# Performance work log

Measured on AMD Instinct MI355X. Metric: run time of the kernel, lower is better.

## Reference

```python
import jax, jax.numpy as jnp
import numpy as np
from jax import lax

DIM = 256
HEAD_DIM = 64          # v head dim and hedgehog dim
HEAD_DIM_QK = 64       # must equal HEAD_DIM for the module to run
NH = DIM // HEAD_DIM   # 4
EPS = 1e-6


def setup_inputs() -> dict:
    key = jax.random.key(0)
    ks = jax.random.split(key, 12)
    B, C, H, W, D = 1, DIM, 16, 16, 16
    x = jax.random.normal(ks[0], (B, C, H, W, D), dtype=jnp.float32)
    qk_dim = HEAD_DIM_QK * NH
    # 1x1x1 conv weights for q, k (qkv_bias=False)
    Wq = jax.random.normal(ks[1], (qk_dim, C), dtype=jnp.float32) * 0.02
    Wk = jax.random.normal(ks[2], (qk_dim, C), dtype=jnp.float32) * 0.02
    # depthwise 3x3x3 conv for v (groups=dim, bias=True)
    Wv = jax.random.normal(ks[3], (C, 1, 3, 3, 3), dtype=jnp.float32) * 0.1
    bv = jax.random.normal(ks[4], (C,), dtype=jnp.float32) * 0.02
    # HedgeHog linear layers (init is identity/zeros; use near-identity + noise)
    eye = jnp.eye(HEAD_DIM, dtype=jnp.float32)
    Wmq = eye * 0.5 + jax.random.normal(ks[5], (HEAD_DIM, HEAD_DIM), dtype=jnp.float32) * 0.02
    bmq = jnp.zeros((HEAD_DIM,), dtype=jnp.float32)
    Wmk = eye * 0.5 + jax.random.normal(ks[6], (HEAD_DIM, HEAD_DIM), dtype=jnp.float32) * 0.02
    bmk = jnp.zeros((HEAD_DIM,), dtype=jnp.float32)
    Wmv = eye * 0.5 + jax.random.normal(ks[7], (HEAD_DIM, HEAD_DIM), dtype=jnp.float32) * 0.02
    bmv = jnp.zeros((HEAD_DIM,), dtype=jnp.float32)
    return {"x": x, "Wq": Wq, "Wk": Wk, "Wv": Wv, "bv": bv,
            "Wmq": Wmq, "bmq": bmq, "Wmk": Wmk, "bmk": bmk,
            "Wmv": Wmv, "bmv": bmv}


def _hedgehog(z, W, b):
    # z: [B, nh, N, d] -> [B, 2*nh, N, d]; cat along HEAD axis (dim=1) as in torch code
    h = jnp.einsum('bhnd,ed->bhne', z, W) + b
    return jnp.concatenate([jnp.exp(h), jnp.exp(-h)], axis=1)


def reference(x, Wq, Wk, Wv, bv, Wmq, bmq, Wmk, bmk, Wmv, bmv):
    B, C, H, W_, D = x.shape
    N = H * W_ * D
    x2 = x.reshape(B, C, N)
    # 1x1x1 conv projections
    q = jnp.einsum('oc,bcn->bon', Wq, x2)  # [B, qk_dim, N]
    k = jnp.einsum('oc,bcn->bon', Wk, x2)
    # depthwise 3x3x3 conv for v
    v3 = lax.conv_general_dilated(
        x, Wv, window_strides=(1, 1, 1),
        padding=((1, 1), (1, 1), (1, 1)),
        dimension_numbers=('NCDHW', 'OIDHW', 'NCDHW'),
        feature_group_count=C) + bv[None, :, None, None, None]
    v = v3.reshape(B, C, N)
    # split heads, tokens-last -> tokens axis
    q1 = q.reshape(B, NH, HEAD_DIM_QK, N).transpose(0, 1, 3, 2)  # [B,nh,N,dqk]
    k1 = k.reshape(B, NH, HEAD_DIM_QK, N).transpose(0, 1, 3, 2)
    v1 = v.reshape(B, NH, HEAD_DIM, N).transpose(0, 1, 3, 2)     # [B,nh,N,dv]
    qf = _hedgehog(q1, Wmq, bmq)  # [B,2nh,N,dqk]
    kf = _hedgehog(k1, Wmk, bmk)
    vf = _hedgehog(v1, Wmv, bmv)  # [B,2nh,N,dv]
    # quadratic "linear" attention: row-sum normalized QK^T
    qk = jnp.einsum('bhmd,bhnd->bhmn', qf, kf)          # [B,2nh,N,N]
    attn = qk / (jnp.sum(qk, axis=-1, keepdims=True) + EPS)
    out = jnp.einsum('bhmn,bhnd->bhmd', attn, vf)        # [B,2nh,N,dv]
    out = out.transpose(0, 1, 3, 2).reshape(B, 2 * C, H, W_, D)
    return out
```

## Files before the change

kernel.cpp:

```cpp
#include <hip/hip_runtime.h>
#include <math.h>

#define EPS_F 1e-6f

#define OFF_WCQ 0
#define OFF_WCK (OFF_WCQ + 65536)
#define OFF_BV  (OFF_WCK + 65536)
#define OFF_VC  (OFF_BV + 256)
#define OFF_PS  (OFF_VC + 256*4096)
#define OFF_PSV (OFF_PS + 8*64*4096)
#define OFF_SM  (OFF_PSV + 8*64*64)
#define OFF_SV  (OFF_SM + 8*4096)

__global__ __launch_bounds__(256) void k_combine(
    const float* __restrict__ Wq, const float* __restrict__ Wk,
    const float* __restrict__ Wmq, const float* __restrict__ Wmk,
    const float* __restrict__ Wmv, const float* __restrict__ bmv,
    const float* __restrict__ bv, float* __restrict__ ws)
{
    int row = blockIdx.x;
    int c = threadIdx.x;
    int h = row >> 6, e = row & 63;
    float aq = 0.f, ak = 0.f;
    for (int d = 0; d < 64; ++d) {
        float mq = Wmq[e*64 + d];
        float mk = Wmk[e*64 + d];
        int src = (h*64 + d)*256 + c;
        aq = fmaf(mq, Wq[src], aq);
        ak = fmaf(mk, Wk[src], ak);
    }
    ws[OFF_WCQ + row*256 + c] = aq;
    ws[OFF_WCK + row*256 + c] = ak;
    if (c == 0) {
        float av = 0.f;
        for (int d = 0; d < 64; ++d) av = fmaf(Wmv[e*64 + d], bv[h*64 + d], av);
        ws[OFF_BV + row] = av + bmv[e];
    }
}

__global__ __launch_bounds__(256) void k_dwconv(
    const float* __restrict__ x, const float* __restrict__ Wv, float* __restrict__ vc)
{
    int c = blockIdx.y;
    int n = blockIdx.x * 256 + threadIdx.x;
    int z = n >> 8, y = (n >> 4) & 15, xx = n & 15;
    const float* xc = x + c * 4096;
    const float* wc = Wv + c * 27;
    float acc = 0.f;
    #pragma unroll
    for (int kz = 0; kz < 3; ++kz) {
        int zz = z + kz - 1;
        if (zz < 0 || zz > 15) continue;
        #pragma unroll
        for (int ky = 0; ky < 3; ++ky) {
            int yy = y + ky - 1;
            if (yy < 0 || yy > 15) continue;
            #pragma unroll
            for (int kx = 0; kx < 3; ++kx) {
                int xv = xx + kx - 1;
                if (xv < 0 || xv > 15) continue;
                acc = fmaf(wc[(kz*3 + ky)*3 + kx], xc[(zz << 8) + (yy << 4) + xv], acc);
            }
        }
    }
    vc[c*4096 + n] = acc;
}

__global__ __launch_bounds__(256, 1) void k_kv_fused(
    const float* __restrict__ X, const float* __restrict__ bmk,
    const float* __restrict__ Wmv, float* __restrict__ ws)
{
    __shared__ float smem[16384];
    float (*Xs)[64]  = (float(*)[64])smem;
    float (*Ws)[68]  = (float(*)[68])(smem + 4096);
    float (*kfp)[64] = (float(*)[64])smem;
    float (*kfm)[64] = (float(*)[64])(smem + 4096);
    float (*vfp)[64] = (float(*)[64])(smem + 8192);
    float (*vfm)[64] = (float(*)[64])(smem + 12288);

    int t = threadIdx.x;
    int chunk = blockIdx.x;
    int hb = blockIdx.y;
    int n0 = chunk * 64;
    int lc = t >> 6, ln = t & 63;
    int e4 = (t & 15) * 4;
    int n4 = (t >> 4) * 4;

    float accK[4][4], accV[4][4];
    #pragma unroll
    for (int i = 0; i < 4; ++i)
        #pragma unroll
        for (int j = 0; j < 4; ++j) { accK[i][j] = 0.f; accV[i][j] = 0.f; }

    const float* Wck = ws + OFF_WCK;
    for (int c0 = 0; c0 < 256; c0 += 64) {
        #pragma unroll
        for (int i = 0; i < 16; ++i)
            Xs[lc*16 + i][ln] = X[(size_t)(c0 + lc*16 + i)*4096 + n0 + ln];
        #pragma unroll
        for (int i = 0; i < 16; ++i)
            Ws[ln][lc*16 + i] = Wck[(size_t)(hb*64 + lc*16 + i)*256 + c0 + ln];
        __syncthreads();
        #pragma unroll 4
        for (int c = 0; c < 64; ++c) {
            float4 xv4 = *(const float4*)&Xs[c][n4];
            float4 wv4 = *(const float4*)&Ws[c][e4];
            float xv[4] = {xv4.x, xv4.y, xv4.z, xv4.w};
            float wv[4] = {wv4.x, wv4.y, wv4.z, wv4.w};
            #pragma unroll
            for (int ii = 0; ii < 4; ++ii)
                #pragma unroll
                for (int jj = 0; jj < 4; ++jj)
                    accK[ii][jj] = fmaf(xv[ii], wv[jj], accK[ii][jj]);
        }
        __syncthreads();
    }

    const float* vcb = ws + OFF_VC + (size_t)hb*64*4096;
    #pragma unroll
    for (int i = 0; i < 16; ++i)
        Xs[lc*16 + i][ln] = vcb[(size_t)(lc*16 + i)*4096 + n0 + ln];
    #pragma unroll
    for (int i = 0; i < 16; ++i) { int idx = i*256 + t; Ws[idx & 63][idx >> 6] = Wmv[idx]; }
    __syncthreads();
    #pragma unroll 4
    for (int d = 0; d < 64; ++d) {
        float4 xv4 = *(const float4*)&Xs[d][n4];
        float4 wv4 = *(const float4*)&Ws[d][e4];
        float xv[4] = {xv4.x, xv4.y, xv4.z, xv4.w};
        float wv[4] = {wv4.x, wv4.y, wv4.z, wv4.w};
        #pragma unroll
        for (int ii = 0; ii < 4; ++ii)
            #pragma unroll
            for (int jj = 0; jj < 4; ++jj)
                accV[ii][jj] = fmaf(xv[ii], wv[jj], accV[ii][jj]);
    }
    __syncthreads();

    float bk[4], bvv[4];
    #pragma unroll
    for (int j = 0; j < 4; ++j) { bk[j] = bmk[e4 + j]; bvv[j] = ws[OFF_BV + hb*64 + e4 + j]; }
    #pragma unroll
    for (int ii = 0; ii < 4; ++ii) {
        float pk[4], mk_[4], pv[4], mv[4];
        #pragma unroll
        for (int jj = 0; jj < 4; ++jj) {
            float a = accK[ii][jj] + bk[jj];
            pk[jj] = __expf(a);  mk_[jj] = __expf(-a);
            float b = accV[ii][jj] + bvv[jj];
            pv[jj] = __expf(b);  mv[jj] = __expf(-b);
        }
        *(float4*)&kfp[n4 + ii][e4] = make_float4(pk[0], pk[1], pk[2], pk[3]);
        *(float4*)&kfm[n4 + ii][e4] = make_float4(mk_[0], mk_[1], mk_[2], mk_[3]);
        *(float4*)&vfp[n4 + ii][e4] = make_float4(pv[0], pv[1], pv[2], pv[3]);
        *(float4*)&vfm[n4 + ii][e4] = make_float4(mv[0], mv[1], mv[2], mv[3]);
    }
    __syncthreads();

    float aSp[4][4], aSm[4][4], svp[4], svm[4];
    #pragma unroll
    for (int i = 0; i < 4; ++i) {
        svp[i] = 0.f; svm[i] = 0.f;
        #pragma unroll
        for (int j = 0; j < 4; ++j) { aSp[i][j] = 0.f; aSm[i][j] = 0.f; }
    }
    int a4 = e4, f4 = n4;
    #pragma unroll 2
    for (int n = 0; n < 64; ++n) {
        float4 kp4 = *(const float4*)&kfp[n][a4];
        float4 km4 = *(const float4*)&kfm[n][a4];
        float4 vp4 = *(const float4*)&vfp[n][f4];
        float4 vm4 = *(const float4*)&vfm[n][f4];
        float kp[4] = {kp4.x, kp4.y, kp4.z, kp4.w};
        float km[4] = {km4.x, km4.y, km4.z, km4.w};
        float vp[4] = {vp4.x, vp4.y, vp4.z, vp4.w};
        float vm[4] = {vm4.x, vm4.y, vm4.z, vm4.w};
        #pragma unroll
        for (int ai = 0; ai < 4; ++ai) {
            svp[ai] += kp[ai];  svm[ai] += km[ai];
            #pragma unroll
            for (int fi = 0; fi < 4; ++fi) {
                aSp[ai][fi] = fmaf(kp[ai], vp[fi], aSp[ai][fi]);
                aSm[ai][fi] = fmaf(km[ai], vm[fi], aSm[ai][fi]);
            }
        }
    }
    float* pSp = ws + OFF_PS + (size_t)(hb*64 + chunk)*4096;
    float* pSm = ws + OFF_PS + (size_t)((hb + 4)*64 + chunk)*4096;
    #pragma unroll
    for (int ai = 0; ai < 4; ++ai) {
        *(float4*)&pSp[(a4 + ai)*64 + f4] = make_float4(aSp[ai][0], aSp[ai][1], aSp[ai][2], aSp[ai][3]);
        *(float4*)&pSm[(a4 + ai)*64 + f4] = make_float4(aSm[ai][0], aSm[ai][1], aSm[ai][2], aSm[ai][3]);
    }
    if (t < 16) {
        float* pvp = ws + OFF_PSV + (size_t)(hb*64 + chunk)*64;
        float* pvm = ws + OFF_PSV + (size_t)((hb + 4)*64 + chunk)*64;
        *(float4*)&pvp[a4] = make_float4(svp[0], svp[1], svp[2], svp[3]);
        *(float4*)&pvm[a4] = make_float4(svm[0], svm[1], svm[2], svm[3]);
    }
}

__global__ __launch_bounds__(256) void k_reduce(float* __restrict__ ws)
{
    int idx = blockIdx.x*256 + threadIdx.x;
    if (idx < 8*4096) {
        int h = idx >> 12, r = idx & 4095;
        float s = 0.f;
        #pragma unroll 16
        for (int c = 0; c < 64; ++c) s += ws[OFF_PS + (size_t)(h*64 + c)*4096 + r];
        ws[OFF_SM + idx] = s;
    } else if (idx < 8*4096 + 512) {
        int j = idx - 8*4096;
        int h = j >> 6, e = j & 63;
        float s = 0.f;
        #pragma unroll 16
        for (int c = 0; c < 64; ++c) s += ws[OFF_PSV + (size_t)(h*64 + c)*64 + e];
        ws[OFF_SV + j] = s;
    }
}

__global__ __launch_bounds__(256, 1) void k_q_out(
    const float* __restrict__ X, const float* __restrict__ bmq,
    const float* __restrict__ ws, float* __restrict__ out)
{
    __shared__ float smem[12352];
    float (*Xs)[64]   = (float(*)[64])smem;
    float (*Wsh)[68]  = (float(*)[68])(smem + 4096);
    float (*qfTp)[64] = (float(*)[64])smem;
    float (*qfTm)[64] = (float(*)[64])(smem + 4096);
    float (*Sms)[64]  = (float(*)[64])(smem + 8192);
    float* svs        = smem + 12288;

    int t = threadIdx.x;
    int chunk = blockIdx.x;
    int hb = blockIdx.y;
    int n0 = chunk * 64;
    int lc = t >> 6, ln = t & 63;
    int a4_1 = (t & 15) * 4;
    int n4_1 = (t >> 4) * 4;

    float accQ[4][4];
    #pragma unroll
    for (int i = 0; i < 4; ++i)
        #pragma unroll
        for (int j = 0; j < 4; ++j) accQ[i][j] = 0.f;

    const float* Wcq = ws + OFF_WCQ;
    for (int c0 = 0; c0 < 256; c0 += 64) {
        #pragma unroll
        for (int i = 0; i < 16; ++i)
            Xs[lc*16 + i][ln] = X[(size_t)(c0 + lc*16 + i)*4096 + n0 + ln];
        #pragma unroll
        for (int i = 0; i < 16; ++i)
            Wsh[ln][lc*16 + i] = Wcq[(size_t)(hb*64 + lc*16 + i)*256 + c0 + ln];
        __syncthreads();
        #pragma unroll 4
        for (int c = 0; c < 64; ++c) {
            float4 xv4 = *(const float4*)&Xs[c][n4_1];
            float4 wv4 = *(const float4*)&Wsh[c][a4_1];
            float xv[4] = {xv4.x, xv4.y, xv4.z, xv4.w};
            float wv[4] = {wv4.x, wv4.y, wv4.z, wv4.w};
            #pragma unroll
            for (int ii = 0; ii < 4; ++ii)
                #pragma unroll
                for (int jj = 0; jj < 4; ++jj)
                    accQ[ii][jj] = fmaf(xv[ii], wv[jj], accQ[ii][jj]);
        }
        __syncthreads();
    }

    #pragma unroll
    for (int jj = 0; jj < 4; ++jj) {
        float b = bmq[a4_1 + jj];
        float v0 = accQ[0][jj] + b, v1 = accQ[1][jj] + b,
              v2 = accQ[2][jj] + b, v3 = accQ[3][jj] + b;
        *(float4*)&qfTp[a4_1 + jj][n4_1] =
            make_float4(__expf(v0), __expf(v1), __expf(v2), __expf(v3));
        *(float4*)&qfTm[a4_1 + jj][n4_1] =
            make_float4(__expf(-v0), __expf(-v1), __expf(-v2), __expf(-v3));
    }

    int n4 = (t & 15) * 4;
    int e4 = (t >> 4) * 4;
    for (int s = 0; s < 2; ++s) {
        int h = hb + 4*s;
        __syncthreads();
        const float* Smg = ws + OFF_SM + (size_t)h*4096;
        #pragma unroll
        for (int i = 0; i < 16; ++i) { int idx = i*256 + t; Sms[idx >> 6][idx & 63] = Smg[idx]; }
        if (t < 64) svs[t] = ws[OFF_SV + h*64 + t];
        __syncthreads();

        const float (*qf)[64] = s ? (const float(*)[64])qfTm : (const float(*)[64])qfTp;
        float acc[4][4];
        float den[4] = {0.f, 0.f, 0.f, 0.f};
        #pragma unroll
        for (int i = 0; i < 4; ++i)
            #pragma unroll
            for (int j = 0; j < 4; ++j) acc[i][j] = 0.f;
        #pragma unroll 4
        for (int a = 0; a < 64; ++a) {
            float4 qv4 = *(const float4*)&qf[a][n4];
            float4 sm4 = *(const float4*)&Sms[a][e4];
            float qv[4] = {qv4.x, qv4.y, qv4.z, qv4.w};
            float sm[4] = {sm4.x, sm4.y, sm4.z, sm4.w};
            float sva = svs[a];
            #pragma unroll
            for (int nj = 0; nj < 4; ++nj) {
                den[nj] = fmaf(qv[nj], sva, den[nj]);
                #pragma unroll
                for (int ei = 0; ei < 4; ++ei)
                    acc[ei][nj] = fmaf(sm[ei], qv[nj], acc[ei][nj]);
            }
        }
        float r[4];
        #pragma unroll
        for (int nj = 0; nj < 4; ++nj) r[nj] = 1.f / (den[nj] + EPS_F);
        #pragma unroll
        for (int ei = 0; ei < 4; ++ei)
            *(float4*)&out[(size_t)(h*64 + e4 + ei)*4096 + n0 + n4] =
                make_float4(acc[ei][0]*r[0], acc[ei][1]*r[1], acc[ei][2]*r[2], acc[ei][3]*r[3]);
    }
}

extern "C" void kernel_launch(void* const* d_in, const int* in_sizes, int n_in,
                              void* d_out, int out_size, void* d_ws, size_t ws_size,
                              hipStream_t stream) {
    const float* x   = (const float*)d_in[0];
    const float* Wq  = (const float*)d_in[1];
    const float* Wk  = (const float*)d_in[2];
    const float* Wv  = (const float*)d_in[3];
    const float* bv  = (const float*)d_in[4];
    const float* Wmq = (const float*)d_in[5];
    const float* bmq = (const float*)d_in[6];
    const float* Wmk = (const float*)d_in[7];
    const float* bmk = (const float*)d_in[8];
    const float* Wmv = (const float*)d_in[9];
    const float* bmv = (const float*)d_in[10];
    float* out = (float*)d_out;
    float* ws  = (float*)d_ws;

    k_combine<<<256, 256, 0, stream>>>(Wq, Wk, Wmq, Wmk, Wmv, bmv, bv, ws);
    k_dwconv<<<dim3(16, 256), 256, 0, stream>>>(x, Wv, ws + OFF_VC);
    k_kv_fused<<<dim3(64, 4), 256, 0, stream>>>(x, bmk, Wmv, ws);
    k_reduce<<<130, 256, 0, stream>>>(ws);
    k_q_out<<<dim3(64, 4), 256, 0, stream>>>(x, bmq, ws, out);
}
```

Before: 148.3 us.

## Fuse Q projection into KV kernel and split output kernel per head

```diff
diff --git a/kernel.cpp b/kernel.cpp
--- a/kernel.cpp
+++ b/kernel.cpp
@@ -11,6 +11,7 @@
 #define OFF_PSV (OFF_PS + 8*64*4096)
 #define OFF_SM  (OFF_PSV + 8*64*64)
 #define OFF_SV  (OFF_SM + 8*4096)
+#define OFF_QF  (OFF_SV + 512)
 
 __global__ __launch_bounds__(256) void k_combine(
     const float* __restrict__ Wq, const float* __restrict__ Wk,
@@ -66,13 +67,15 @@
     vc[c*4096 + n] = acc;
 }
 
-__global__ __launch_bounds__(256, 1) void k_kv_fused(
+__global__ __launch_bounds__(512, 2) void k_fused(
     const float* __restrict__ X, const float* __restrict__ bmk,
-    const float* __restrict__ Wmv, float* __restrict__ ws)
+    const float* __restrict__ bmq, const float* __restrict__ Wmv,
+    float* __restrict__ ws)
 {
     __shared__ float smem[16384];
     float (*Xs)[64]  = (float(*)[64])smem;
-    float (*Ws)[68]  = (float(*)[68])(smem + 4096);
+    float (*Wsk)[68] = (float(*)[68])(smem + 4096);
+    float (*Wsq)[68] = (float(*)[68])(smem + 8448);
     float (*kfp)[64] = (float(*)[64])smem;
     float (*kfm)[64] = (float(*)[64])(smem + 4096);
     float (*vfp)[64] = (float(*)[64])(smem + 8192);
@@ -82,78 +85,107 @@
     int chunk = blockIdx.x;
     int hb = blockIdx.y;
     int n0 = chunk * 64;
-    int lc = t >> 6, ln = t & 63;
-    int e4 = (t & 15) * 4;
-    int n4 = (t >> 4) * 4;
-
-    float accK[4][4], accV[4][4];
+    bool isQ = (t >= 256);
+    int tl = t & 255;
+    int lc = tl >> 6, ln = tl & 63;
+    int e4 = (tl & 15) * 4;
+    int n4 = (tl >> 4) * 4;
+
+    float acc[4][4];
+    float accV[4][4];
     #pragma unroll
     for (int i = 0; i < 4; ++i)
         #pragma unroll
-        for (int j = 0; j < 4; ++j) { accK[i][j] = 0.f; accV[i][j] = 0.f; }
+        for (int j = 0; j < 4; ++j) { acc[i][j] = 0.f; accV[i][j] = 0.f; }
 
     const float* Wck = ws + OFF_WCK;
+    const float* Wcq = ws + OFF_WCQ;
     for (int c0 = 0; c0 < 256; c0 += 64) {
-        #pragma unroll
-        for (int i = 0; i < 16; ++i)
-            Xs[lc*16 + i][ln] = X[(size_t)(c0 + lc*16 + i)*4096 + n0 + ln];
-        #pragma unroll
-        for (int i = 0; i < 16; ++i)
-            Ws[ln][lc*16 + i] = Wck[(size_t)(hb*64 + lc*16 + i)*256 + c0 + ln];
+        if (!isQ) {
+            #pragma unroll
+            for (int i = 0; i < 16; ++i)
+                Xs[lc*16 + i][ln] = X[(size_t)(c0 + lc*16 + i)*4096 + n0 + ln];
+        } else {
+            #pragma unroll
+            for (int i = 0; i < 16; ++i) {
+                Wsk[ln][lc*16 + i] = Wck[(size_t)(hb*64 + lc*16 + i)*256 + c0 + ln];
+                Wsq[ln][lc*16 + i] = Wcq[(size_t)(hb*64 + lc*16 + i)*256 + c0 + ln];
+            }
+        }
         __syncthreads();
+        const float (*Wsh)[68] = isQ ? (const float (*)[68])Wsq : (const float (*)[68])Wsk;
         #pragma unroll 4
         for (int c = 0; c < 64; ++c) {
             float4 xv4 = *(const float4*)&Xs[c][n4];
-            float4 wv4 = *(const float4*)&Ws[c][e4];
+            float4 wv4 = *(const float4*)&Wsh[c][e4];
             float xv[4] = {xv4.x, xv4.y, xv4.z, xv4.w};
             float wv[4] = {wv4.x, wv4.y, wv4.z, wv4.w};
             #pragma unroll
             for (int ii = 0; ii < 4; ++ii)
                 #pragma unroll
                 for (int jj = 0; jj < 4; ++jj)
-                    accK[ii][jj] = fmaf(xv[ii], wv[jj], accK[ii][jj]);
+                    acc[ii][jj] = fmaf(xv[ii], wv[jj], acc[ii][jj]);
         }
         __syncthreads();
     }
 
-    const float* vcb = ws + OFF_VC + (size_t)hb*64*4096;
-    #pragma unroll
-    for (int i = 0; i < 16; ++i)
-        Xs[lc*16 + i][ln] = vcb[(size_t)(lc*16 + i)*4096 + n0 + ln];
-    #pragma unroll
-    for (int i = 0; i < 16; ++i) { int idx = i*256 + t; Ws[idx & 63][idx >> 6] = Wmv[idx]; }
-    __syncthreads();
-    #pragma unroll 4
-    for (int d = 0; d < 64; ++d) {
-        float4 xv4 = *(const float4*)&Xs[d][n4];
-        float4 wv4 = *(const float4*)&Ws[d][e4];
-        float xv[4] = {xv4.x, xv4.y, xv4.z, xv4.w};
-        float wv[4] = {wv4.x, wv4.y, wv4.z, wv4.w};
-        #pragma unroll
-        for (int ii = 0; ii < 4; ++ii)
-            #pragma unroll
-            for (int jj = 0; jj < 4; ++jj)
-                accV[ii][jj] = fmaf(xv[ii], wv[jj], accV[ii][jj]);
-    }
-    __syncthreads();
-
-    float bk[4], bvv[4];
-    #pragma unroll
-    for (int j = 0; j < 4; ++j) { bk[j] = bmk[e4 + j]; bvv[j] = ws[OFF_BV + hb*64 + e4 + j]; }
-    #pragma unroll
-    for (int ii = 0; ii < 4; ++ii) {
-        float pk[4], mk_[4], pv[4], mv[4];
+    if (!isQ) {
+        const float* vcb = ws + OFF_VC + (size_t)hb*64*4096;
+        #pragma unroll
+        for (int i = 0; i < 16; ++i)
+            Xs[lc*16 + i][ln] = vcb[(size_t)(lc*16 + i)*4096 + n0 + ln];
+        #pragma unroll
+        for (int i = 0; i < 16; ++i) { int idx = i*256 + tl; Wsk[idx & 63][idx >> 6] = Wmv[idx]; }
+    } else {
+        float* gq = ws + OFF_QF;
         #pragma unroll
         for (int jj = 0; jj < 4; ++jj) {
-            float a = accK[ii][jj] + bk[jj];
-            pk[jj] = __expf(a);  mk_[jj] = __expf(-a);
-            float b = accV[ii][jj] + bvv[jj];
-            pv[jj] = __expf(b);  mv[jj] = __expf(-b);
-        }
-        *(float4*)&kfp[n4 + ii][e4] = make_float4(pk[0], pk[1], pk[2], pk[3]);
-        *(float4*)&kfm[n4 + ii][e4] = make_float4(mk_[0], mk_[1], mk_[2], mk_[3]);
-        *(float4*)&vfp[n4 + ii][e4] = make_float4(pv[0], pv[1], pv[2], pv[3]);
-        *(float4*)&vfm[n4 + ii][e4] = make_float4(mv[0], mv[1], mv[2], mv[3]);
+            float b = bmq[e4 + jj];
+            float a0 = acc[0][jj] + b, a1 = acc[1][jj] + b,
+                  a2 = acc[2][jj] + b, a3 = acc[3][jj] + b;
+            *(float4*)&gq[(size_t)(hb*64 + e4 + jj)*4096 + n0 + n4] =
+                make_float4(__expf(a0), __expf(a1), __expf(a2), __expf(a3));
+            *(float4*)&gq[(size_t)((hb + 4)*64 + e4 + jj)*4096 + n0 + n4] =
+                make_float4(__expf(-a0), __expf(-a1), __expf(-a2), __expf(-a3));
+        }
+    }
+    __syncthreads();
+
+    if (!isQ) {
+        #pragma unroll 4
+        for (int d = 0; d < 64; ++d) {
+            float4 xv4 = *(const float4*)&Xs[d][n4];
+            float4 wv4 = *(const float4*)&Wsk[d][e4];
+            float xv[4] = {xv4.x, xv4.y, xv4.z, xv4.w};
+            float wv[4] = {wv4.x, wv4.y, wv4.z, wv4.w};
+            #pragma unroll
+            for (int ii = 0; ii < 4; ++ii)
+                #pragma unroll
+                for (int jj = 0; jj < 4; ++jj)
+                    accV[ii][jj] = fmaf(xv[ii], wv[jj], accV[ii][jj]);
+        }
+    }
+    __syncthreads();
+
+    if (!isQ) {
+        float bk[4], bvv[4];
+        #pragma unroll
+        for (int j = 0; j < 4; ++j) { bk[j] = bmk[e4 + j]; bvv[j] = ws[OFF_BV + hb*64 + e4 + j]; }
+        #pragma unroll
+        for (int ii = 0; ii < 4; ++ii) {
+            float pk[4], mk_[4], pv[4], mv[4];
+            #pragma unroll
+            for (int jj = 0; jj < 4; ++jj) {
+                float a = acc[ii][jj] + bk[jj];
+                pk[jj] = __expf(a);  mk_[jj] = __expf(-a);
+                float b = accV[ii][jj] + bvv[jj];
+                pv[jj] = __expf(b);  mv[jj] = __expf(-b);
+            }
+            *(float4*)&kfp[n4 + ii][e4] = make_float4(pk[0], pk[1], pk[2], pk[3]);
+            *(float4*)&kfm[n4 + ii][e4] = make_float4(mk_[0], mk_[1], mk_[2], mk_[3]);
+            *(float4*)&vfp[n4 + ii][e4] = make_float4(pv[0], pv[1], pv[2], pv[3]);
+            *(float4*)&vfm[n4 + ii][e4] = make_float4(mv[0], mv[1], mv[2], mv[3]);
+        }
     }
     __syncthreads();
 
@@ -165,8 +197,10 @@
         for (int j = 0; j < 4; ++j) { aSp[i][j] = 0.f; aSm[i][j] = 0.f; }
     }
     int a4 = e4, f4 = n4;
+    int nb = isQ ? 32 : 0;
     #pragma unroll 2
-    for (int n = 0; n < 64; ++n) {
+    for (int nn = 0; nn < 32; ++nn) {
+        int n = nb + nn;
         float4 kp4 = *(const float4*)&kfp[n][a4];
         float4 km4 = *(const float4*)&kfm[n][a4];
         float4 vp4 = *(const float4*)&vfp[n][f4];
@@ -185,18 +219,51 @@
             }
         }
     }
-    float* pSp = ws + OFF_PS + (size_t)(hb*64 + chunk)*4096;
-    float* pSm = ws + OFF_PS + (size_t)((hb + 4)*64 + chunk)*4096;
-    #pragma unroll
-    for (int ai = 0; ai < 4; ++ai) {
-        *(float4*)&pSp[(a4 + ai)*64 + f4] = make_float4(aSp[ai][0], aSp[ai][1], aSp[ai][2], aSp[ai][3]);
-        *(float4*)&pSm[(a4 + ai)*64 + f4] = make_float4(aSm[ai][0], aSm[ai][1], aSm[ai][2], aSm[ai][3]);
-    }
-    if (t < 16) {
-        float* pvp = ws + OFF_PSV + (size_t)(hb*64 + chunk)*64;
-        float* pvm = ws + OFF_PSV + (size_t)((hb + 4)*64 + chunk)*64;
-        *(float4*)&pvp[a4] = make_float4(svp[0], svp[1], svp[2], svp[3]);
-        *(float4*)&pvm[a4] = make_float4(svm[0], svm[1], svm[2], svm[3]);
+    __syncthreads();
+
+    if (isQ) {
+        #pragma unroll
+        for (int i = 0; i < 4; ++i)
+            #pragma unroll
+            for (int j = 0; j < 4; ++j) {
+                smem[(i*4 + j)*256 + tl]        = aSp[i][j];
+                smem[(16 + i*4 + j)*256 + tl]   = aSm[i][j];
+            }
+        if (tl < 16) {
+            #pragma unroll
+            for (int i = 0; i < 4; ++i) {
+                smem[8192 + i*16 + tl]      = svp[i];
+                smem[8192 + 64 + i*16 + tl] = svm[i];
+            }
+        }
+    }
+    __syncthreads();
+    if (!isQ) {
+        #pragma unroll
+        for (int i = 0; i < 4; ++i)
+            #pragma unroll
+            for (int j = 0; j < 4; ++j) {
+                aSp[i][j] += smem[(i*4 + j)*256 + tl];
+                aSm[i][j] += smem[(16 + i*4 + j)*256 + tl];
+            }
+        float* pSp = ws + OFF_PS + (size_t)(hb*64 + chunk)*4096;
+        float* pSm = ws + OFF_PS + (size_t)((hb + 4)*64 + chunk)*4096;
+        #pragma unroll
+        for (int ai = 0; ai < 4; ++ai) {
+            *(float4*)&pSp[(a4 + ai)*64 + f4] = make_float4(aSp[ai][0], aSp[ai][1], aSp[ai][2], aSp[ai][3]);
+            *(float4*)&pSm[(a4 + ai)*64 + f4] = make_float4(aSm[ai][0], aSm[ai][1], aSm[ai][2], aSm[ai][3]);
+        }
+        if (tl < 16) {
+            #pragma unroll
+            for (int i = 0; i < 4; ++i) {
+                svp[i] += smem[8192 + i*16 + tl];
+                svm[i] += smem[8192 + 64 + i*16 + tl];
+            }
+            float* pvp = ws + OFF_PSV + (size_t)(hb*64 + chunk)*64;
+            float* pvm = ws + OFF_PSV + (size_t)((hb + 4)*64 + chunk)*64;
+            *(float4*)&pvp[a4] = make_float4(svp[0], svp[1], svp[2], svp[3]);
+            *(float4*)&pvm[a4] = make_float4(svm[0], svm[1], svm[2], svm[3]);
+        }
     }
 }
 
@@ -219,108 +286,58 @@
     }
 }
 
-__global__ __launch_bounds__(256, 1) void k_q_out(
-    const float* __restrict__ X, const float* __restrict__ bmq,
+__global__ __launch_bounds__(256, 2) void k_out(
     const float* __restrict__ ws, float* __restrict__ out)
 {
-    __shared__ float smem[12352];
-    float (*Xs)[64]   = (float(*)[64])smem;
-    float (*Wsh)[68]  = (float(*)[68])(smem + 4096);
-    float (*qfTp)[64] = (float(*)[64])smem;
-    float (*qfTm)[64] = (float(*)[64])(smem + 4096);
-    float (*Sms)[64]  = (float(*)[64])(smem + 8192);
-    float* svs        = smem + 12288;
-
+    __shared__ float qs[64][64];
+    __shared__ float Sms[64][64];
+    __shared__ float svs[64];
     int t = threadIdx.x;
     int chunk = blockIdx.x;
-    int hb = blockIdx.y;
+    int h = blockIdx.y;
     int n0 = chunk * 64;
     int lc = t >> 6, ln = t & 63;
-    int a4_1 = (t & 15) * 4;
-    int n4_1 = (t >> 4) * 4;
-
-    float accQ[4][4];
-    #pragma unroll
-    for (int i = 0; i < 4; ++i)
-        #pragma unroll
-        for (int j = 0; j < 4; ++j) accQ[i][j] = 0.f;
-
-    const float* Wcq = ws + OFF_WCQ;
-    for (int c0 = 0; c0 < 256; c0 += 64) {
-        #pragma unroll
-        for (int i = 0; i < 16; ++i)
-            Xs[lc*16 + i][ln] = X[(size_t)(c0 + lc*16 + i)*4096 + n0 + ln];
-        #pragma unroll
-        for (int i = 0; i < 16; ++i)
-            Wsh[ln][lc*16 + i] = Wcq[(size_t)(hb*64 + lc*16 + i)*256 + c0 + ln];
-        __syncthreads();
-        #pragma unroll 4
-        for (int c = 0; c < 64; ++c) {
-            float4 xv4 = *(const float4*)&Xs[c][n4_1];
-            float4 wv4 = *(const float4*)&Wsh[c][a4_1];
-            float xv[4] = {xv4.x, xv4.y, xv4.z, xv4.w};
-            float wv[4] = {wv4.x, wv4.y, wv4.z, wv4.w};
-            #pragma unroll
-            for (int ii = 0; ii < 4; ++ii)
-                #pragma unroll
-                for (int jj = 0; jj < 4; ++jj)
-                    accQ[ii][jj] = fmaf(xv[ii], wv[jj], accQ[ii][jj]);
-        }
-        __syncthreads();
-    }
-
-    #pragma unroll
-    for (int jj = 0; jj < 4; ++jj) {
-        float b = bmq[a4_1 + jj];
-        float v0 = accQ[0][jj] + b, v1 = accQ[1][jj] + b,
-              v2 = accQ[2][jj] + b, v3 = accQ[3][jj] + b;
-        *(float4*)&qfTp[a4_1 + jj][n4_1] =
-            make_float4(__expf(v0), __expf(v1), __expf(v2), __expf(v3));
-        *(float4*)&qfTm[a4_1 + jj][n4_1] =
-            make_float4(__expf(-v0), __expf(-v1), __expf(-v2), __expf(-v3));
-    }
+
+    const float* gq = ws + OFF_QF + (size_t)h*64*4096;
+    #pragma unroll
+    for (int i = 0; i < 16; ++i)
+        qs[lc*16 + i][ln] = gq[(size_t)(lc*16 + i)*4096 + n0 + ln];
+    const float* Smg = ws + OFF_SM + (size_t)h*4096;
+    #pragma unroll
+    for (int i = 0; i < 16; ++i) { int idx = i*256 + t; Sms[idx >> 6][idx & 63] = Smg[idx]; }
+    if (t < 64) svs[t] = ws[OFF_SV + h*64 + t];
+    __syncthreads();
 
     int n4 = (t & 15) * 4;
     int e4 = (t >> 4) * 4;
-    for (int s = 0; s < 2; ++s) {
-        int h = hb + 4*s;
-        __syncthreads();
-        const float* Smg = ws + OFF_SM + (size_t)h*4096;
-        #pragma unroll
-        for (int i = 0; i < 16; ++i) { int idx = i*256 + t; Sms[idx >> 6][idx & 63] = Smg[idx]; }
-        if (t < 64) svs[t] = ws[OFF_SV + h*64 + t];
-        __syncthreads();
-
-        const float (*qf)[64] = s ? (const float(*)[64])qfTm : (const float(*)[64])qfTp;
-        float acc[4][4];
-        float den[4] = {0.f, 0.f, 0.f, 0.f};
-        #pragma unroll
-        for (int i = 0; i < 4; ++i)
-            #pragma unroll
-            for (int j = 0; j < 4; ++j) acc[i][j] = 0.f;
-        #pragma unroll 4
-        for (int a = 0; a < 64; ++a) {
-            float4 qv4 = *(const float4*)&qf[a][n4];
-            float4 sm4 = *(const float4*)&Sms[a][e4];
-            float qv[4] = {qv4.x, qv4.y, qv4.z, qv4.w};
-            float sm[4] = {sm4.x, sm4.y, sm4.z, sm4.w};
-            float sva = svs[a];
-            #pragma unroll
-            for (int nj = 0; nj < 4; ++nj) {
-                den[nj] = fmaf(qv[nj], sva, den[nj]);
-                #pragma unroll
-                for (int ei = 0; ei < 4; ++ei)
-                    acc[ei][nj] = fmaf(sm[ei], qv[nj], acc[ei][nj]);
-            }
-        }
-        float r[4];
-        #pragma unroll
-        for (int nj = 0; nj < 4; ++nj) r[nj] = 1.f / (den[nj] + EPS_F);
-        #pragma unroll
-        for (int ei = 0; ei < 4; ++ei)
-            *(float4*)&out[(size_t)(h*64 + e4 + ei)*4096 + n0 + n4] =
-                make_float4(acc[ei][0]*r[0], acc[ei][1]*r[1], acc[ei][2]*r[2], acc[ei][3]*r[3]);
-    }
+    float acc[4][4];
+    float den[4] = {0.f, 0.f, 0.f, 0.f};
+    #pragma unroll
+    for (int i = 0; i < 4; ++i)
+        #pragma unroll
+        for (int j = 0; j < 4; ++j) acc[i][j] = 0.f;
+    #pragma unroll 4
+    for (int a = 0; a < 64; ++a) {
+        float4 qv4 = *(const float4*)&qs[a][n4];
+        float4 sm4 = *(const float4*)&Sms[a][e4];
+        float qv[4] = {qv4.x, qv4.y, qv4.z, qv4.w};
+        float sm[4] = {sm4.x, sm4.y, sm4.z, sm4.w};
+        float sva = svs[a];
+        #pragma unroll
+        for (int nj = 0; nj < 4; ++nj) {
+            den[nj] = fmaf(qv[nj], sva, den[nj]);
+            #pragma unroll
+            for (int ei = 0; ei < 4; ++ei)
+                acc[ei][nj] = fmaf(sm[ei], qv[nj], acc[ei][nj]);
+        }
+    }
+    float r[4];
+    #pragma unroll
+    for (int nj = 0; nj < 4; ++nj) r[nj] = 1.f / (den[nj] + EPS_F);
+    #pragma unroll
+    for (int ei = 0; ei < 4; ++ei)
+        *(float4*)&out[(size_t)(h*64 + e4 + ei)*4096 + n0 + n4] =
+            make_float4(acc[ei][0]*r[0], acc[ei][1]*r[1], acc[ei][2]*r[2], acc[ei][3]*r[3]);
 }
 
 extern "C" void kernel_launch(void* const* d_in, const int* in_sizes, int n_in,
@@ -342,7 +359,7 @@
 
     k_combine<<<256, 256, 0, stream>>>(Wq, Wk, Wmq, Wmk, Wmv, bmv, bv, ws);
     k_dwconv<<<dim3(16, 256), 256, 0, stream>>>(x, Wv, ws + OFF_VC);
-    k_kv_fused<<<dim3(64, 4), 256, 0, stream>>>(x, bmk, Wmv, ws);
+    k_fused<<<dim3(64, 4), 512, 0, stream>>>(x, bmk, bmq, Wmv, ws);
     k_reduce<<<130, 256, 0, stream>>>(ws);
-    k_q_out<<<dim3(64, 4), 256, 0, stream>>>(x, bmq, ws, out);
-}
+    k_out<<<dim3(64, 8), 256, 0, stream>>>(ws, out);
+}
```

Result: faster. 140.7 us (-5.1%).
